# Kernel optimization log

Measured on AMD Instinct MI355X. Metric: run time of the kernel, lower is better.

Reference implementation:

```python
import jax, jax.numpy as jnp
import numpy as np

B, H, L, V = 128, 1024, 60, 50257


def setup_inputs() -> dict:
    key = jax.random.key(0)
    ks = jax.random.split(key, 14)
    s = 0.02
    f32 = jnp.float32
    return {
        "input": jax.random.randint(ks[0], (B,), 0, V),
        "hidden": jax.random.normal(ks[1], (1, B, H), f32),
        "encoder_outputs": jax.random.normal(ks[2], (B, L, H), f32),
        # learned parameters
        "emb": (jax.random.normal(ks[3], (V, H), f32) * s),
        "attn_W": (jax.random.normal(ks[4], (L, 2 * H), f32) * s),
        "attn_b": jnp.zeros((L,), f32),
        "comb_W": (jax.random.normal(ks[5], (H, 2 * H), f32) * s),
        "comb_b": jnp.zeros((H,), f32),
        "W_ih": (jax.random.normal(ks[6], (3 * H, H), f32) * s),
        "W_hh": (jax.random.normal(ks[7], (3 * H, H), f32) * s),
        "b_ih": jnp.zeros((3 * H,), f32),
        "b_hh": jnp.zeros((3 * H,), f32),
        "out_W": (jax.random.normal(ks[8], (V, H), f32) * s),
        "out_b": jnp.zeros((V,), f32),
    }


def reference(input, hidden, encoder_outputs, emb, attn_W, attn_b,
              comb_W, comb_b, W_ih, W_hh, b_ih, b_hh, out_W, out_b):
    # embedding lookup (dropout is identity in eval mode)
    embedded = emb[input]                      # [B, H]
    h = hidden[0]                              # [B, H]

    # Bahdanau-style attention over fixed max_length positions
    attn_logits = jnp.concatenate([embedded, h], axis=1) @ attn_W.T + attn_b  # [B, L]
    attn_weights = jax.nn.softmax(attn_logits, axis=1)                        # [B, L]
    attn_applied = jnp.einsum('bl,blh->bh', attn_weights, encoder_outputs)    # [B, H]

    # combine + relu
    x = jnp.concatenate([embedded, attn_applied], axis=1) @ comb_W.T + comb_b  # [B, H]
    x = jax.nn.relu(x)

    # single GRU step (PyTorch gate order: r, z, n)
    gi = x @ W_ih.T + b_ih                     # [B, 3H]
    gh = h @ W_hh.T + b_hh                     # [B, 3H]
    i_r, i_z, i_n = jnp.split(gi, 3, axis=1)
    h_r, h_z, h_n = jnp.split(gh, 3, axis=1)
    r = jax.nn.sigmoid(i_r + h_r)
    z = jax.nn.sigmoid(i_z + h_z)
    n = jnp.tanh(i_n + r * h_n)
    h_new = (1.0 - z) * n + z * h              # [B, H]

    # output projection + log_softmax over vocab
    logp = jax.nn.log_softmax(h_new @ out_W.T + out_b, axis=1)  # [B, V]
    return logp, h_new[None], attn_weights
```

## Files before the change

### kernel.cpp

```cpp
#include <hip/hip_runtime.h>
#include <hip/hip_bf16.h>

#define B_ 128
#define H_ 1024
#define L_ 60
#define V_ 50257

typedef __attribute__((ext_vector_type(8))) short bf16x8;
typedef __attribute__((ext_vector_type(4))) float f32x4;

__device__ __forceinline__ unsigned short f2bf(float f) {
  union { __hip_bfloat16 h; unsigned short u; } v;
  v.h = __float2bfloat16(f);
  return v.u;
}

__device__ __forceinline__ bf16x8 cvt8(float4 a, float4 b) {
  union { bf16x8 v; __hip_bfloat16 h[8]; } u;
  u.h[0] = __float2bfloat16(a.x); u.h[1] = __float2bfloat16(a.y);
  u.h[2] = __float2bfloat16(a.z); u.h[3] = __float2bfloat16(a.w);
  u.h[4] = __float2bfloat16(b.x); u.h[5] = __float2bfloat16(b.y);
  u.h[6] = __float2bfloat16(b.z); u.h[7] = __float2bfloat16(b.w);
  return u.v;
}

__device__ __forceinline__ void gl_lds16(const void* g, void* l) {
  __builtin_amdgcn_global_load_lds(
      (const __attribute__((address_space(1))) unsigned int*)g,
      (__attribute__((address_space(3))) unsigned int*)l, 16, 0, 0);
}

#define SBAR()   __builtin_amdgcn_s_barrier()
#define SCHED0() __builtin_amdgcn_sched_barrier(0)
__device__ __forceinline__ void vwait4() { asm volatile("s_waitcnt vmcnt(4)" ::: "memory"); }
__device__ __forceinline__ void vwait0() { asm volatile("s_waitcnt vmcnt(0)" ::: "memory"); }

__device__ __forceinline__ size_t packIdx(int b, int k) {
  int s = k >> 5;
  int bm = b >> 4;
  int lane = (b & 15) | (((k >> 3) & 3) << 4);
  return ((size_t)((s * 8 + bm) * 64 + lane) << 3) | (size_t)(k & 7);
}

__global__ __launch_bounds__(256) void k_embh(
    const int* __restrict__ input, const float* __restrict__ hidden,
    const float* __restrict__ emb, unsigned short* __restrict__ aXa,
    unsigned short* __restrict__ aH)
{
  int idx = blockIdx.x * 256 + threadIdx.x;
  int b = idx >> 10, j = idx & (H_ - 1);
  float e = emb[(size_t)input[b] * H_ + j];
  float h = hidden[idx];
  size_t p = packIdx(b, j);
  aXa[p] = f2bf(e);
  aH[p]  = f2bf(h);
}

__global__ __launch_bounds__(256) void k_alog(
    const int* __restrict__ input, const float* __restrict__ hidden,
    const float* __restrict__ emb, const float* __restrict__ attn_W,
    const float* __restrict__ attn_b, float* __restrict__ lbuf)
{
  int t = threadIdx.x, wv = t >> 6, lane = t & 63;
  int task = blockIdx.x * 4 + wv;
  int b = task / L_, l = task - b * L_;
  const float* erow = emb + (size_t)input[b] * H_;
  const float* hrow = hidden + (size_t)b * H_;
  const float* wr = attn_W + (size_t)l * (2 * H_);
  float acc = 0.f;
  #pragma unroll 4
  for (int i = 0; i < 16; ++i) {
    int m = lane + i * 64;
    acc += erow[m] * wr[m] + hrow[m] * wr[H_ + m];
  }
  #pragma unroll
  for (int off = 32; off; off >>= 1) acc += __shfl_xor(acc, off);
  if (lane == 0) lbuf[b * 64 + l] = acc + attn_b[l];
}

__global__ __launch_bounds__(256) void k_asm(
    const float* __restrict__ lbuf, float* __restrict__ attnw,
    float* __restrict__ wbuf)
{
  int t = threadIdx.x, wv = t >> 6, lane = t & 63;
  int b = blockIdx.x * 4 + wv;
  float v = (lane < L_) ? lbuf[b * 64 + lane] : -1e30f;
  float m = v;
  #pragma unroll
  for (int off = 32; off; off >>= 1) m = fmaxf(m, __shfl_xor(m, off));
  float e = (lane < L_) ? __expf(v - m) : 0.f;
  float s = e;
  #pragma unroll
  for (int off = 32; off; off >>= 1) s += __shfl_xor(s, off);
  float w = e / s;
  if (lane < L_) { attnw[b * L_ + lane] = w; wbuf[b * 64 + lane] = w; }
}

__global__ __launch_bounds__(256) void k_app(
    const float* __restrict__ enc, const float* __restrict__ wbuf,
    unsigned short* __restrict__ aXa)
{
  __shared__ float sWt[64];
  int b = blockIdx.x, q = blockIdx.y, t = threadIdx.x;
  if (t < L_) sWt[t] = wbuf[b * 64 + t];
  __syncthreads();
  int col = q * 256 + t;
  const float* eb = enc + (size_t)b * L_ * H_ + col;
  float acc = 0.f;
  #pragma unroll 4
  for (int l = 0; l < L_; ++l) acc += sWt[l] * eb[(size_t)l * H_];
  aXa[packIdx(b, H_ + col)] = f2bf(acc);
}

__global__ __launch_bounds__(256) void k_gemm(
    const unsigned short* __restrict__ Apk, const unsigned short* __restrict__ Apk2,
    const float* __restrict__ Wt, const float* __restrict__ Wt2,
    const float* __restrict__ bias, float* __restrict__ Cdir,
    float* __restrict__ Cpart, float* __restrict__ Cpart2,
    float* __restrict__ pms, int K, int N, int nchunks, int halfY, int nblkx)
{
  __shared__ __align__(16) float bufW[2][64 * 32];
  __shared__ __align__(16) unsigned short bufA[2][128 * 32];
  int t = threadIdx.x, wv = t >> 6, lane = t & 63;
  int y = blockIdx.y;
  const unsigned short* A = Apk;
  const float* W = Wt;
  float* CP = Cpart;
  int sidx = y;
  if (halfY && y >= halfY) { A = Apk2; W = Wt2; CP = Cpart2; sidx = y - halfY; }
  int chunk0 = sidx * nchunks;
  int n0 = blockIdx.x * 64;
  int bm0 = wv * 2;
  int srow8 = lane >> 3;
  int sch = lane & 7;

  f32x4 acc[2][4];
  #pragma unroll
  for (int i = 0; i < 2; ++i)
    #pragma unroll
    for (int j = 0; j < 4; ++j) acc[i][j] = (f32x4){0.f, 0.f, 0.f, 0.f};

  auto STAGE = [&](int kc, int bi) {
    #pragma unroll
    for (int i = 0; i < 2; ++i) {
      int r = wv * 16 + i * 8 + srow8;
      int gcol = n0 + r; gcol = (gcol < N) ? gcol : (N - 1);
      int c = sch ^ (r & 7);
      const float* src = W + (size_t)gcol * K + (size_t)kc * 32 + c * 4;
      gl_lds16(src, &bufW[bi][(wv * 16 + i * 8) * 32]);
    }
    #pragma unroll
    for (int j = 0; j < 2; ++j) {
      const unsigned short* src = A + ((size_t)kc * 8 + bm0 + j) * 512 + lane * 8;
      gl_lds16(src, &bufA[bi][(bm0 + j) * 512]);
    }
  };

  STAGE(chunk0, 0);
  STAGE(chunk0 + 1, 1);
  vwait4(); SCHED0(); SBAR();

  int g = lane >> 4;
  for (int kk = 0; kk < nchunks; ++kk) {
    const float* bw = bufW[kk & 1];
    const unsigned short* ba = bufA[kk & 1];
    bf16x8 a0 = *(const bf16x8*)&ba[(bm0) * 512 + lane * 8];
    bf16x8 a1 = *(const bf16x8*)&ba[(bm0 + 1) * 512 + lane * 8];
    #pragma unroll
    for (int nc = 0; nc < 4; ++nc) {
      int rr = nc * 16 + (lane & 15);
      int c0 = (g * 2) ^ (rr & 7);
      int c1 = (g * 2 + 1) ^ (rr & 7);
      float4 w0 = *(const float4*)&bw[rr * 32 + c0 * 4];
      float4 w1 = *(const float4*)&bw[rr * 32 + c1 * 4];
      bf16x8 bfr = cvt8(w0, w1);
      acc[0][nc] = __builtin_amdgcn_mfma_f32_16x16x32_bf16(a0, bfr, acc[0][nc], 0, 0, 0);
      acc[1][nc] = __builtin_amdgcn_mfma_f32_16x16x32_bf16(a1, bfr, acc[1][nc], 0, 0, 0);
    }
    if (kk + 1 < nchunks) {
      SCHED0(); SBAR();
      if (kk + 2 < nchunks) { STAGE(chunk0 + kk + 2, kk & 1); vwait4(); }
      else                  { vwait0(); }
      SCHED0(); SBAR();
    }
  }

  int cols[4]; float bv[4];
  #pragma unroll
  for (int nc = 0; nc < 4; ++nc) {
    int c = n0 + nc * 16 + (lane & 15);
    cols[nc] = c;
    bv[nc] = (bias && c < N) ? bias[c] : 0.f;
  }
  int rb = (lane >> 4) * 4;
  if (CP) {
    float* dst = CP + (size_t)sidx * B_ * N;
    #pragma unroll
    for (int bm = 0; bm < 2; ++bm)
      #pragma unroll
      for (int r = 0; r < 4; ++r) {
        int row = (bm0 + bm) * 16 + rb + r;
        #pragma unroll
        for (int nc = 0; nc < 4; ++nc)
          if (cols[nc] < N) dst[(size_t)row * N + cols[nc]] = acc[bm][nc][r];
      }
  } else {
    #pragma unroll
    for (int bm = 0; bm < 2; ++bm)
      #pragma unroll
      for (int r = 0; r < 4; ++r) {
        int row = (bm0 + bm) * 16 + rb + r;
        #pragma unroll
        for (int nc = 0; nc < 4; ++nc)
          if (cols[nc] < N) Cdir[(size_t)row * N + cols[nc]] = acc[bm][nc][r] + bv[nc];
      }
    if (pms) {
      #pragma unroll
      for (int bm = 0; bm < 2; ++bm)
        #pragma unroll
        for (int r = 0; r < 4; ++r) {
          int row = (bm0 + bm) * 16 + rb + r;
          float m = -1e30f;
          #pragma unroll
          for (int nc = 0; nc < 4; ++nc)
            if (cols[nc] < N) m = fmaxf(m, acc[bm][nc][r] + bv[nc]);
          #pragma unroll
          for (int off = 8; off; off >>= 1) m = fmaxf(m, __shfl_xor(m, off));
          float e = 0.f;
          #pragma unroll
          for (int nc = 0; nc < 4; ++nc)
            if (cols[nc] < N) e += __expf(acc[bm][nc][r] + bv[nc] - m);
          #pragma unroll
          for (int off = 8; off; off >>= 1) e += __shfl_xor(e, off);
          if ((lane & 15) == 0) {
            size_t o = ((size_t)row * nblkx + blockIdx.x) * 2;
            pms[o] = m; pms[o + 1] = e;
          }
        }
    }
  }
}

__global__ __launch_bounds__(256) void k_reduce_comb(
    const float* __restrict__ parts, const float* __restrict__ bias,
    unsigned short* __restrict__ aX)
{
  int idx = blockIdx.x * 256 + threadIdx.x;
  int b = idx >> 10, j = idx & (H_ - 1);
  float s = bias[j];
  #pragma unroll
  for (int p = 0; p < 8; ++p) s += parts[(size_t)p * B_ * H_ + idx];
  s = fmaxf(s, 0.f);
  aX[packIdx(b, j)] = f2bf(s);
}

__global__ __launch_bounds__(256) void k_gate(
    const float* __restrict__ giP, const float* __restrict__ ghP,
    const float* __restrict__ b_ih, const float* __restrict__ b_hh,
    const float* __restrict__ hidden, float* __restrict__ hnew,
    unsigned short* __restrict__ aHn)
{
  int idx = blockIdx.x * 256 + threadIdx.x;
  int b = idx >> 10, j = idx & (H_ - 1);
  size_t base = (size_t)b * 3 * H_;
  float ir = b_ih[j], iz = b_ih[H_ + j], in_ = b_ih[2 * H_ + j];
  float hr = b_hh[j], hz = b_hh[H_ + j], hn = b_hh[2 * H_ + j];
  #pragma unroll
  for (int p = 0; p < 4; ++p) {
    const float* gi = giP + (size_t)p * B_ * 3 * H_ + base;
    const float* gh = ghP + (size_t)p * B_ * 3 * H_ + base;
    ir += gi[j]; iz += gi[H_ + j]; in_ += gi[2 * H_ + j];
    hr += gh[j]; hz += gh[H_ + j]; hn += gh[2 * H_ + j];
  }
  float r = 1.f / (1.f + __expf(-(ir + hr)));
  float z = 1.f / (1.f + __expf(-(iz + hz)));
  float n = tanhf(in_ + r * hn);
  float h = hidden[idx];
  float hv = (1.f - z) * n + z * h;
  hnew[idx] = hv;
  aHn[packIdx(b, j)] = f2bf(hv);
}

__global__ __launch_bounds__(256) void k_lsmr(
    const float* __restrict__ pms, float* __restrict__ cbuf, int nblk)
{
  __shared__ float sm[4], ss[4];
  int b = blockIdx.x, t = threadIdx.x;
  float M = -1e30f, S = 0.f;
  for (int i = t; i < nblk; i += 256) {
    float m = pms[((size_t)b * nblk + i) * 2];
    float s = pms[((size_t)b * nblk + i) * 2 + 1];
    float nm = fmaxf(M, m);
    S = S * __expf(M - nm) + s * __expf(m - nm);
    M = nm;
  }
  #pragma unroll
  for (int off = 32; off; off >>= 1) {
    float m2 = __shfl_xor(M, off), s2 = __shfl_xor(S, off);
    float nm = fmaxf(M, m2);
    S = S * __expf(M - nm) + s2 * __expf(m2 - nm);
    M = nm;
  }
  if ((t & 63) == 0) { sm[t >> 6] = M; ss[t >> 6] = S; }
  __syncthreads();
  if (t == 0) {
    float Mf = sm[0], Sf = ss[0];
    #pragma unroll
    for (int i = 1; i < 4; ++i) {
      float nm = fmaxf(Mf, sm[i]);
      Sf = Sf * __expf(Mf - nm) + ss[i] * __expf(sm[i] - nm);
      Mf = nm;
    }
    cbuf[b] = Mf + logf(Sf);
  }
}

#define SL_ 6283
__global__ __launch_bounds__(256) void k_lsub(
    float* __restrict__ logits, const float* __restrict__ cbuf)
{
  int b = blockIdx.x, sl = blockIdx.y, t = threadIdx.x;
  float c = cbuf[b];
  int v0 = sl * SL_;
  int v1 = v0 + SL_; if (v1 > V_) v1 = V_;
  float* row = logits + (size_t)b * V_;
  for (int v = v0 + t; v < v1; v += 256) row[v] -= c;
}

extern "C" void kernel_launch(void* const* d_in, const int* in_sizes, int n_in,
                              void* d_out, int out_size, void* d_ws, size_t ws_size,
                              hipStream_t stream)
{
  const int*   input  = (const int*)d_in[0];
  const float* hidden = (const float*)d_in[1];
  const float* enc    = (const float*)d_in[2];
  const float* emb    = (const float*)d_in[3];
  const float* attn_W = (const float*)d_in[4];
  const float* attn_b = (const float*)d_in[5];
  const float* comb_W = (const float*)d_in[6];
  const float* comb_b = (const float*)d_in[7];
  const float* W_ih   = (const float*)d_in[8];
  const float* W_hh   = (const float*)d_in[9];
  const float* b_ih   = (const float*)d_in[10];
  const float* b_hh   = (const float*)d_in[11];
  const float* out_W  = (const float*)d_in[12];
  const float* out_b  = (const float*)d_in[13];

  float* out    = (float*)d_out;
  float* logits = out;
  float* hnew   = out + (size_t)B_ * V_;
  float* attnw  = hnew + (size_t)B_ * H_;

  const int NBLK = (V_ + 63) / 64;
  char* ws = (char*)d_ws;
  unsigned short* aXa = (unsigned short*)(ws);
  unsigned short* aH  = (unsigned short*)(ws + 524288);
  unsigned short* aX  = (unsigned short*)(ws + 786432);
  unsigned short* aHn = (unsigned short*)(ws + 1048576);
  float* wbuf  = (float*)(ws + 1310720);
  float* lbuf  = (float*)(ws + 1343488);
  float* cbuf  = (float*)(ws + 1376256);
  float* pms   = (float*)(ws + 1380352);
  float* combP = (float*)(ws + 2185216);
  float* giP   = (float*)(ws + 6379520);
  float* ghP   = (float*)(ws + 12670976);

  k_embh<<<512, 256, 0, stream>>>(input, hidden, emb, aXa, aH);
  k_alog<<<(B_ * L_) / 4, 256, 0, stream>>>(input, hidden, emb, attn_W, attn_b, lbuf);
  k_asm<<<B_ / 4, 256, 0, stream>>>(lbuf, attnw, wbuf);
  k_app<<<dim3(B_, 4), 256, 0, stream>>>(enc, wbuf, aXa);
  k_gemm<<<dim3(16, 8), 256, 0, stream>>>(aXa, nullptr, comb_W, nullptr, nullptr,
                                          nullptr, combP, nullptr, nullptr,
                                          2 * H_, H_, 8, 0, 0);
  k_reduce_comb<<<(B_ * H_) / 256, 256, 0, stream>>>(combP, comb_b, aX);
  k_gemm<<<dim3(48, 8), 256, 0, stream>>>(aX, aH, W_ih, W_hh, nullptr,
                                          nullptr, giP, ghP, nullptr,
                                          H_, 3 * H_, 8, 4, 0);
  k_gate<<<(B_ * H_) / 256, 256, 0, stream>>>(giP, ghP, b_ih, b_hh, hidden, hnew, aHn);
  k_gemm<<<dim3(NBLK, 1), 256, 0, stream>>>(aHn, nullptr, out_W, nullptr, out_b,
                                            logits, nullptr, nullptr, pms,
                                            H_, V_, 32, 0, NBLK);
  k_lsmr<<<B_, 256, 0, stream>>>(pms, cbuf, NBLK);
  k_lsub<<<dim3(B_, 8), 256, 0, stream>>>(logits, cbuf);
}
```

Measured before the change: 133.6 us.

## Triple-buffer GEMM staging, split comb GEMM deeper, fuse logsumexp into subtract

The GEMM main loop moves from a double to a triple LDS buffer. This allows a single barrier per chunk, with the next-next stage issued before compute instead of two barriers after it. The combine GEMM now splits K into 16 partitions of 4 chunks for more blocks, and the reduction sums 16 partials to match. The row logsumexp reduction is folded into the subtract kernel, so each of the 8 slices recomputes it, removing one launch in exchange for redundant reads of the partial max/sum buffer. Workspace offsets are compacted so gi/gh partials alias the comb partials buffer.

Result: slower. 147.9 us (+10.7%).

```diff
diff --git a/kernel.cpp b/kernel.cpp
--- a/kernel.cpp
+++ b/kernel.cpp
@@ -119,8 +119,8 @@
     float* __restrict__ Cpart, float* __restrict__ Cpart2,
     float* __restrict__ pms, int K, int N, int nchunks, int halfY, int nblkx)
 {
-  __shared__ __align__(16) float bufW[2][64 * 32];
-  __shared__ __align__(16) unsigned short bufA[2][128 * 32];
+  __shared__ __align__(16) float bufW[3][64 * 32];
+  __shared__ __align__(16) unsigned short bufA[3][128 * 32];
   int t = threadIdx.x, wv = t >> 6, lane = t & 63;
   int y = blockIdx.y;
   const unsigned short* A = Apk;
@@ -158,12 +158,18 @@
 
   STAGE(chunk0, 0);
   STAGE(chunk0 + 1, 1);
-  vwait4(); SCHED0(); SBAR();
 
   int g = lane >> 4;
+  int bi = 0;
   for (int kk = 0; kk < nchunks; ++kk) {
-    const float* bw = bufW[kk & 1];
-    const unsigned short* ba = bufA[kk & 1];
+    if (kk < nchunks - 1) vwait4(); else vwait0();
+    SCHED0(); SBAR(); SCHED0();
+    if (kk + 2 < nchunks) {
+      int bi2 = bi + 2; if (bi2 >= 3) bi2 -= 3;
+      STAGE(chunk0 + kk + 2, bi2);
+    }
+    const float* bw = bufW[bi];
+    const unsigned short* ba = bufA[bi];
     bf16x8 a0 = *(const bf16x8*)&ba[(bm0) * 512 + lane * 8];
     bf16x8 a1 = *(const bf16x8*)&ba[(bm0 + 1) * 512 + lane * 8];
     #pragma unroll
@@ -177,12 +183,7 @@
       acc[0][nc] = __builtin_amdgcn_mfma_f32_16x16x32_bf16(a0, bfr, acc[0][nc], 0, 0, 0);
       acc[1][nc] = __builtin_amdgcn_mfma_f32_16x16x32_bf16(a1, bfr, acc[1][nc], 0, 0, 0);
     }
-    if (kk + 1 < nchunks) {
-      SCHED0(); SBAR();
-      if (kk + 2 < nchunks) { STAGE(chunk0 + kk + 2, kk & 1); vwait4(); }
-      else                  { vwait0(); }
-      SCHED0(); SBAR();
-    }
+    bi = (bi == 2) ? 0 : bi + 1;
   }
 
   int cols[4]; float bv[4];
@@ -249,7 +250,7 @@
   int b = idx >> 10, j = idx & (H_ - 1);
   float s = bias[j];
   #pragma unroll
-  for (int p = 0; p < 8; ++p) s += parts[(size_t)p * B_ * H_ + idx];
+  for (int p = 0; p < 16; ++p) s += parts[(size_t)p * B_ * H_ + idx];
   s = fmaxf(s, 0.f);
   aX[packIdx(b, j)] = f2bf(s);
 }
@@ -281,11 +282,12 @@
   aHn[packIdx(b, j)] = f2bf(hv);
 }
 
-__global__ __launch_bounds__(256) void k_lsmr(
-    const float* __restrict__ pms, float* __restrict__ cbuf, int nblk)
-{
-  __shared__ float sm[4], ss[4];
-  int b = blockIdx.x, t = threadIdx.x;
+#define SL_ 6283
+__global__ __launch_bounds__(256) void k_lsub(
+    float* __restrict__ logits, const float* __restrict__ pms, int nblk)
+{
+  __shared__ float sm[4], ss[4], sc;
+  int b = blockIdx.x, sl = blockIdx.y, t = threadIdx.x;
   float M = -1e30f, S = 0.f;
   for (int i = t; i < nblk; i += 256) {
     float m = pms[((size_t)b * nblk + i) * 2];
@@ -311,16 +313,10 @@
       Sf = Sf * __expf(Mf - nm) + ss[i] * __expf(sm[i] - nm);
       Mf = nm;
     }
-    cbuf[b] = Mf + logf(Sf);
-  }
-}
-
-#define SL_ 6283
-__global__ __launch_bounds__(256) void k_lsub(
-    float* __restrict__ logits, const float* __restrict__ cbuf)
-{
-  int b = blockIdx.x, sl = blockIdx.y, t = threadIdx.x;
-  float c = cbuf[b];
+    sc = Mf + logf(Sf);
+  }
+  __syncthreads();
+  float c = sc;
   int v0 = sl * SL_;
   int v1 = v0 + SL_; if (v1 > V_) v1 = V_;
   float* row = logits + (size_t)b * V_;
@@ -359,19 +355,18 @@
   unsigned short* aHn = (unsigned short*)(ws + 1048576);
   float* wbuf  = (float*)(ws + 1310720);
   float* lbuf  = (float*)(ws + 1343488);
-  float* cbuf  = (float*)(ws + 1376256);
-  float* pms   = (float*)(ws + 1380352);
+  float* pms   = (float*)(ws + 1376256);
   float* combP = (float*)(ws + 2185216);
-  float* giP   = (float*)(ws + 6379520);
-  float* ghP   = (float*)(ws + 12670976);
+  float* giP   = (float*)(ws + 2185216);
+  float* ghP   = (float*)(ws + 2185216 + 6291456);
 
   k_embh<<<512, 256, 0, stream>>>(input, hidden, emb, aXa, aH);
   k_alog<<<(B_ * L_) / 4, 256, 0, stream>>>(input, hidden, emb, attn_W, attn_b, lbuf);
   k_asm<<<B_ / 4, 256, 0, stream>>>(lbuf, attnw, wbuf);
   k_app<<<dim3(B_, 4), 256, 0, stream>>>(enc, wbuf, aXa);
-  k_gemm<<<dim3(16, 8), 256, 0, stream>>>(aXa, nullptr, comb_W, nullptr, nullptr,
-                                          nullptr, combP, nullptr, nullptr,
-                                          2 * H_, H_, 8, 0, 0);
+  k_gemm<<<dim3(16, 16), 256, 0, stream>>>(aXa, nullptr, comb_W, nullptr, nullptr,
+                                           nullptr, combP, nullptr, nullptr,
+                                           2 * H_, H_, 4, 0, 0);
   k_reduce_comb<<<(B_ * H_) / 256, 256, 0, stream>>>(combP, comb_b, aX);
   k_gemm<<<dim3(48, 8), 256, 0, stream>>>(aX, aH, W_ih, W_hh, nullptr,
                                           nullptr, giP, ghP, nullptr,
@@ -380,6 +375,5 @@
   k_gemm<<<dim3(NBLK, 1), 256, 0, stream>>>(aHn, nullptr, out_W, nullptr, out_b,
                                             logits, nullptr, nullptr, pms,
                                             H_, V_, 32, 0, NBLK);
-  k_lsmr<<<B_, 256, 0, stream>>>(pms, cbuf, NBLK);
-  k_lsub<<<dim3(B_, 8), 256, 0, stream>>>(logits, cbuf);
-}
+  k_lsub<<<dim3(B_, 8), 256, 0, stream>>>(logits, pms, NBLK);
+}
```
